# Kernel optimization log

Measured on AMD Instinct MI355X. Metric: run time of the kernel, lower is better.

Reference implementation:

```python
import jax, jax.numpy as jnp
import numpy as np

# dims: batch, time, d_model, d_state, experts, top-k, expert hidden, regime, layers
B, T, D, S, E, K, H, R, L = 4, 512, 384, 32, 6, 2, 512, 5, 2
DI = 2 * D          # d_inner = expand * d_model
DTR = D // 16       # dt_rank = 24


def setup_inputs() -> dict:
    key = jax.random.key(0)
    ks = iter(jax.random.split(key, 48))
    def nrm(shape, s=0.02):
        return jax.random.normal(next(ks), shape, jnp.float32) * s
    inp = {}
    inp["x"] = jax.random.normal(next(ks), (B, T, D), jnp.float32)
    r = jax.random.uniform(next(ks), (B, R), jnp.float32)
    inp["regime"] = r / r.sum(-1, keepdims=True)  # regime posterior
    # FiLM conditioner
    inp["film_w1"] = nrm((R, D)); inp["film_b1"] = jnp.zeros((D,), jnp.float32)
    inp["film_w2"] = nrm((D, 2 * D)); inp["film_b2"] = jnp.zeros((2 * D,), jnp.float32)
    # SelectiveSSMBlock params, stacked over L layers
    inp["ssm_ng"] = jnp.ones((L, D), jnp.float32); inp["ssm_nb"] = jnp.zeros((L, D), jnp.float32)
    inp["in_w"] = nrm((L, D, 2 * DI))
    inp["xp_w"] = nrm((L, DI, DTR + 2 * S))
    inp["dt_w"] = nrm((L, DTR, DI)); inp["dt_b"] = jnp.zeros((L, DI), jnp.float32)
    inp["a_log_real"] = jnp.log(jnp.clip(-0.5 * jax.random.normal(next(ks), (L, DI, S), jnp.float32), 1e-4, None))
    inp["a_imag"] = 0.1 * jax.random.normal(next(ks), (L, DI, S), jnp.float32)
    inp["ssm_d"] = jnp.ones((L, DI), jnp.float32)
    inp["out_w"] = nrm((L, DI, D))
    # MoELayer params, stacked over L layers
    inp["moe_ng"] = jnp.ones((L, D), jnp.float32); inp["moe_nb"] = jnp.zeros((L, D), jnp.float32)
    inp["r_w1"] = nrm((L, D + R, D)); inp["r_b1"] = jnp.zeros((L, D), jnp.float32)
    inp["r_w2"] = nrm((L, D, E)); inp["r_b2"] = jnp.zeros((L, E), jnp.float32)
    inp["e_w1"] = nrm((L, E, D, H)); inp["e_b1"] = jnp.zeros((L, E, H), jnp.float32)
    inp["e_w2"] = nrm((L, E, H, D)); inp["e_b2"] = jnp.zeros((L, E, D), jnp.float32)
    # final norm
    inp["fin_g"] = jnp.ones((D,), jnp.float32); inp["fin_b"] = jnp.zeros((D,), jnp.float32)
    return inp


def _ln(x, g, b):
    m = x.mean(-1, keepdims=True)
    v = ((x - m) ** 2).mean(-1, keepdims=True)
    return (x - m) * jax.lax.rsqrt(v + 1e-5) * g + b


def _ssm_block(h, ng, nb, in_w, xp_w, dt_w, dt_b, alr, aim, d_vec, out_w):
    B_, T_, _ = h.shape
    xn = _ln(h, ng, nb)
    xz = xn @ in_w                        # (B,T,2*DI)
    x_ssm, z = xz[..., :DI], xz[..., DI:]
    x_dbl = x_ssm @ xp_w                  # (B,T,DTR+2S)
    dt = jax.nn.softplus(x_dbl[..., :DTR] @ dt_w + dt_b)   # (B,T,DI)
    Bp = x_dbl[..., DTR:DTR + S]          # (B,T,S)
    Cp = x_dbl[..., DTR + S:]             # (B,T,S)
    A = (-jnp.exp(alr) + 1j * aim).astype(jnp.complex64)   # (DI,S)

    def step(hc, inp):
        dt_t, bt, ct, xt = inp            # (B,DI),(B,S),(B,S),(B,DI)
        dA = jnp.exp(A[None] * dt_t[:, :, None])                       # (B,DI,S) complex
        hc = dA * hc + ((dt_t * xt)[:, :, None] * bt[:, None, :]).astype(jnp.complex64)
        # (h*C).sum(-1).real == (h.real*C).sum(-1) since C is real
        y = jnp.einsum('bds,bs->bd', hc.real, ct)
        return hc, y

    h0 = jnp.zeros((B_, DI, S), jnp.complex64)
    xsT = (jnp.moveaxis(dt, 1, 0), jnp.moveaxis(Bp, 1, 0),
           jnp.moveaxis(Cp, 1, 0), jnp.moveaxis(x_ssm, 1, 0))
    _, ysT = jax.lax.scan(step, h0, xsT)
    y = jnp.moveaxis(ysT, 0, 1) + d_vec * x_ssm   # skip term D*x
    y = y * jax.nn.silu(z)
    return h + y @ out_w                  # residual (dropout=0)


def _moe(h, regime, ng, nb, rw1, rb1, rw2, rb2, ew1, eb1, ew2, eb2):
    xn = _ln(h, ng, nb)
    B_, T_, _ = xn.shape
    reg = jnp.broadcast_to(regime[:, None, :], (B_, T_, R))
    ri = jnp.concatenate([xn, reg], -1)
    gl = jax.nn.silu(ri @ rw1 + rb1) @ rw2 + rb2    # (B,T,E)
    tv, ti = jax.lax.top_k(gl, K)
    tw = jax.nn.softmax(tv, -1)
    eo = jax.nn.silu(jnp.einsum('btd,edh->bteh', xn, ew1) + eb1)
    eo = jnp.einsum('bteh,ehd->bted', eo, ew2) + eb2   # (B,T,E,D)
    sel = jnp.take_along_axis(eo, ti[..., None], axis=2)  # (B,T,K,D)
    out = (sel * tw[..., None]).sum(2)
    gp = jax.nn.softmax(gl, -1)
    avg_p = gp.mean((0, 1))
    avg_m = jax.nn.one_hot(ti[..., 0], E, dtype=gl.dtype).mean((0, 1))
    aux = 0.01 * E * (avg_p * avg_m).sum()
    return h + out, aux


def reference(x, regime, film_w1, film_b1, film_w2, film_b2, ssm_ng, ssm_nb, in_w,
              xp_w, dt_w, dt_b, a_log_real, a_imag, ssm_d, out_w, moe_ng, moe_nb,
              r_w1, r_b1, r_w2, r_b2, e_w1, e_b1, e_w2, e_b2, fin_g, fin_b):
    # FiLM conditioning from regime posterior
    gb = jax.nn.silu(regime @ film_w1 + film_b1) @ film_w2 + film_b2
    gamma, beta = gb[:, :D], gb[:, D:]
    h = x * (gamma[:, None, :] + 1.0) + beta[:, None, :]
    aux = jnp.float32(0.0)
    for l in range(L):
        h = _ssm_block(h, ssm_ng[l], ssm_nb[l], in_w[l], xp_w[l], dt_w[l], dt_b[l],
                       a_log_real[l], a_imag[l], ssm_d[l], out_w[l])
        h, a = _moe(h, regime, moe_ng[l], moe_nb[l], r_w1[l], r_b1[l], r_w2[l], r_b2[l],
                    e_w1[l], e_b1[l], e_w2[l], e_b2[l])
        aux = aux + a
    out = _ln(h, fin_g, fin_b)
    return out, aux
```

## Files before the change

kernel.cpp:

```cpp
#include <hip/hip_runtime.h>
#include <hip/hip_bf16.h>
#include <math.h>

#define B_   4
#define T_   512
#define D_   384
#define S_   32
#define E_   6
#define H_   512
#define R_   5
#define L_   2
#define DI_  768
#define DTR_ 24
#define BT_  2048
#define XPN_ 88
#define SCH  64
#define PIT  40
#define SPD  10
#define SPB  66

typedef short s8v __attribute__((ext_vector_type(8)));
typedef float f32x4 __attribute__((ext_vector_type(4)));
typedef ushort u16x8 __attribute__((ext_vector_type(8)));

__device__ __forceinline__ float siluf(float x) { return x / (1.f + __expf(-x)); }
__device__ __forceinline__ ushort f2b(float f) {
    unsigned u = __float_as_uint(f);
    return (ushort)((u + 0x7FFFu + ((u >> 16) & 1u)) >> 16);
}
__device__ __forceinline__ float b2f(ushort h) { return __uint_as_float(((unsigned)h) << 16); }

#define CN0 1179648L
#define CN1 135168L
#define CN2 36864L
#define CN3 589824L
#define CN4 2359296L
#define CN5 2359296L
#define CN6 294912L
__global__ void conv_k(const float* __restrict__ in_w, const float* __restrict__ xp_w,
                       const float* __restrict__ dt_w, const float* __restrict__ out_w,
                       const float* __restrict__ e_w1, const float* __restrict__ e_w2,
                       const float* __restrict__ r_w1,
                       ushort* __restrict__ in_wb, ushort* __restrict__ xp_wb,
                       ushort* __restrict__ dt_wb, ushort* __restrict__ out_wb,
                       ushort* __restrict__ e1b, ushort* __restrict__ e2b,
                       ushort* __restrict__ r1h, ushort* __restrict__ r1l)
{
    const long total = CN0 + CN1 + CN2 + CN3 + CN4 + CN5 + CN6;
    long stride = (long)gridDim.x * 256;
    for (long i = (long)blockIdx.x * 256 + threadIdx.x; i < total; i += stride) {
        long j = i;
        if (j < CN0) { in_wb[j] = f2b(in_w[j]); continue; }
        j -= CN0;
        if (j < CN1) { xp_wb[j] = f2b(xp_w[j]); continue; }
        j -= CN1;
        if (j < CN2) { dt_wb[j] = f2b(dt_w[j]); continue; }
        j -= CN2;
        if (j < CN3) { out_wb[j] = f2b(out_w[j]); continue; }
        j -= CN3;
        if (j < CN4) { e1b[j] = f2b(e_w1[j]); continue; }
        j -= CN4;
        if (j < CN5) { e2b[j] = f2b(e_w2[j]); continue; }
        j -= CN5;
        {
            long l = j / 147456, rem = j - l * 147456;
            float v = r_w1[l * (long)((D_ + R_) * D_) + rem];
            ushort hv = f2b(v);
            r1h[j] = hv;
            r1l[j] = f2b(v - b2f(hv));
        }
    }
}

__global__ void film_k(const float* __restrict__ regime, const float* __restrict__ w1,
                       const float* __restrict__ b1, const float* __restrict__ w2,
                       const float* __restrict__ b2, float* __restrict__ gb,
                       float* __restrict__ stats)
{
    int b = blockIdx.x;
    int tid = threadIdx.x;
    if (b == 0 && tid < 40) stats[tid] = 0.f;
    __shared__ float t1[D_];
    if (tid < D_) {
        float a = b1[tid];
        for (int r = 0; r < R_; r++) a += regime[b * R_ + r] * w1[r * D_ + tid];
        t1[tid] = siluf(a);
    }
    __syncthreads();
    float a = b2[tid];
    for (int d = 0; d < D_; d++) a += t1[d] * w2[d * (2 * D_) + tid];
    gb[b * (2 * D_) + tid] = a;
}

__global__ void film_apply_k(const float* __restrict__ x, const float* __restrict__ gb,
                             float* __restrict__ h)
{
    int i = blockIdx.x * 256 + threadIdx.x;
    if (i >= B_ * T_ * D_) return;
    int b = i / (T_ * D_);
    int d = i % D_;
    h[i] = x[i] * (1.f + gb[b * (2 * D_) + d]) + gb[b * (2 * D_) + D_ + d];
}

template<int MODE>
__global__ __launch_bounds__(256) void ln_k(const float* __restrict__ in,
                                            const float* __restrict__ g, const float* __restrict__ b,
                                            float* __restrict__ outF,
                                            ushort* __restrict__ outH, ushort* __restrict__ outL)
{
    int row = blockIdx.x;
    int tid = threadIdx.x;
    const float* x = in + (size_t)row * D_;
    float v0 = x[tid];
    float v1 = (tid < D_ - 256) ? x[256 + tid] : 0.f;
    float s = v0 + v1, ss = v0 * v0 + v1 * v1;
#pragma unroll
    for (int o = 32; o > 0; o >>= 1) { s += __shfl_xor(s, o); ss += __shfl_xor(ss, o); }
    __shared__ float sb[8];
    int w = tid >> 6;
    if ((tid & 63) == 0) { sb[w] = s; sb[4 + w] = ss; }
    __syncthreads();
    s = sb[0] + sb[1] + sb[2] + sb[3];
    ss = sb[4] + sb[5] + sb[6] + sb[7];
    float mean = s * (1.f / D_);
    float var = ss * (1.f / D_) - mean * mean;
    float rstd = rsqrtf(var + 1e-5f);
#pragma unroll
    for (int p = 0; p < 2; p++) {
        int c = tid + p * 256;
        if (c >= D_) break;
        float v = (p ? v1 : v0);
        float o = (v - mean) * rstd * g[c] + b[c];
        size_t idx = (size_t)row * D_ + c;
        if (MODE == 0) outF[idx] = o;
        else {
            ushort hv = f2b(o);
            outH[idx] = hv;
            if (MODE == 2) outL[idx] = f2b(o - b2f(hv));
        }
    }
}

template<int MODE>
__global__ __launch_bounds__(256) void selln_k(float* __restrict__ h,
                                               const ushort* __restrict__ eodb,
                                               const float* __restrict__ tw,
                                               const int* __restrict__ tpos,
                                               const float* __restrict__ g, const float* __restrict__ b,
                                               float* __restrict__ outF,
                                               ushort* __restrict__ outH, ushort* __restrict__ outL)
{
    int row = blockIdx.x;
    int tid = threadIdx.x;
    float* hp = h + (size_t)row * D_;
    int p0 = tpos[row * 2], p1 = tpos[row * 2 + 1];
    float w0 = tw[row * 2], w1 = tw[row * 2 + 1];
    const ushort* e0 = eodb + (size_t)p0 * D_;
    const ushort* e1 = eodb + (size_t)p1 * D_;
    float v0 = hp[tid] + w0 * b2f(e0[tid]) + w1 * b2f(e1[tid]);
    float v1 = 0.f;
    if (tid < D_ - 256) v1 = hp[256 + tid] + w0 * b2f(e0[256 + tid]) + w1 * b2f(e1[256 + tid]);
    hp[tid] = v0;
    if (tid < D_ - 256) hp[256 + tid] = v1;
    float s = v0 + v1, ss = v0 * v0 + v1 * v1;
#pragma unroll
    for (int o = 32; o > 0; o >>= 1) { s += __shfl_xor(s, o); ss += __shfl_xor(ss, o); }
    __shared__ float sb[8];
    int w = tid >> 6;
    if ((tid & 63) == 0) { sb[w] = s; sb[4 + w] = ss; }
    __syncthreads();
    s = sb[0] + sb[1] + sb[2] + sb[3];
    ss = sb[4] + sb[5] + sb[6] + sb[7];
    float mean = s * (1.f / D_);
    float var = ss * (1.f / D_) - mean * mean;
    float rstd = rsqrtf(var + 1e-5f);
#pragma unroll
    for (int p = 0; p < 2; p++) {
        int c = tid + p * 256;
        if (c >= D_) break;
        float v = (p ? v1 : v0);
        float o = (v - mean) * rstd * g[c] + b[c];
        size_t idx = (size_t)row * D_ + c;
        if (MODE == 0) outF[idx] = o;
        else {
            ushort hv = f2b(o);
            outH[idx] = hv;
            if (MODE == 2) outL[idx] = f2b(o - b2f(hv));
        }
    }
}

template<int OM, bool NG, bool KG, bool GATHER>
__global__ __launch_bounds__(256) void gemm_b(
    const ushort* __restrict__ A, int lda, long aOff,
    const ushort* __restrict__ W, int ldw, long wOff,
    float* __restrict__ C, int ldc, long cOff,
    ushort* __restrict__ Cb, int ldcb, long cbOff, int nb16,
    const float* __restrict__ bias, long bOff,
    const int* __restrict__ glist, const int* __restrict__ gcnt,
    int N, int K, int act, int acc)
{
    __shared__ __align__(16) ushort As[2][64 * PIT];
    __shared__ __align__(16) ushort Bs[2][64 * PIT];
    const int z = blockIdx.z;
    const int bm = blockIdx.y * 64, bn = blockIdx.x * 64;
    int cnt = 0;
    if (gcnt) { cnt = gcnt[z]; if (bm >= cnt) return; }
    const int tid = threadIdx.x, w = tid >> 6, lane = tid & 63;
    const int wm = (w >> 1) * 32, wn = (w & 1) * 32;
    const int l16 = lane & 15, lk = lane >> 4;
    const int r0 = tid >> 2, c0 = (tid & 3) * 8;
    const ushort* Ab;
    if (GATHER) {
        int gr = bm + r0;
        int t_idx = (gr < cnt) ? glist[(size_t)z * BT_ + gr] : 0;
        Ab = A + (size_t)t_idx * lda;
    } else {
        Ab = A + (size_t)z * aOff + (size_t)(bm + r0) * lda;
    }
    const ushort* Wb = W + (size_t)z * wOff;

    f32x4 accv[2][2];
#pragma unroll
    for (int i = 0; i < 2; i++)
#pragma unroll
        for (int j = 0; j < 2; j++) accv[i][j] = (f32x4)0.f;

    u16x8 arg;
    ushort wrg[8];
    auto LOADA = [&](int k0) {
        arg = *reinterpret_cast<const u16x8*>(Ab + k0 + c0);
    };
    auto LOADW = [&](int k0) {
#pragma unroll
        for (int i = 0; i < 8; i++) {
            int kk = k0 + w * 8 + i;
            bool ok = (!KG || kk < K) && (!NG || (bn + lane) < N);
            wrg[i] = ok ? Wb[(size_t)kk * ldw + bn + lane] : (ushort)0;
        }
    };
    auto STORE = [&](int buf) {
        *reinterpret_cast<u16x8*>(&As[buf][r0 * PIT + c0]) = arg;
        *reinterpret_cast<ushort4*>(&Bs[buf][lane * PIT + w * 8]) =
            make_ushort4(wrg[0], wrg[1], wrg[2], wrg[3]);
        *reinterpret_cast<ushort4*>(&Bs[buf][lane * PIT + w * 8 + 4]) =
            make_ushort4(wrg[4], wrg[5], wrg[6], wrg[7]);
    };

    LOADA(0); LOADW(0); STORE(0);
    __syncthreads();
    const int NIT = (K + 31) / 32;
    for (int it = 0; it < NIT; it++) {
        int cur = it & 1;
        bool more = (it + 1 < NIT);
        if (more) { LOADA((it + 1) * 32); LOADW((it + 1) * 32); }
        s8v af[2], bfr[2];
#pragma unroll
        for (int mf = 0; mf < 2; mf++)
            af[mf] = *reinterpret_cast<const s8v*>(&As[cur][(wm + mf * 16 + l16) * PIT + lk * 8]);
#pragma unroll
        for (int nf = 0; nf < 2; nf++)
            bfr[nf] = *reinterpret_cast<const s8v*>(&Bs[cur][(wn + nf * 16 + l16) * PIT + lk * 8]);
#pragma unroll
        for (int mf = 0; mf < 2; mf++)
#pragma unroll
            for (int nf = 0; nf < 2; nf++)
                accv[mf][nf] = __builtin_amdgcn_mfma_f32_16x16x32_bf16(af[mf], bfr[nf], accv[mf][nf], 0, 0, 0);
        if (more) { STORE(cur ^ 1); __syncthreads(); }
    }

    const float* biasb = bias ? bias + (size_t)z * bOff : nullptr;
#pragma unroll
    for (int mf = 0; mf < 2; mf++) {
#pragma unroll
        for (int nf = 0; nf < 2; nf++) {
            int col = bn + wn + nf * 16 + l16;
            if (NG && col >= N) continue;
#pragma unroll
            for (int r = 0; r < 4; r++) {
                int rr = bm + wm + mf * 16 + lk * 4 + r;
                if (gcnt && rr >= cnt) continue;
                float v = accv[mf][nf][r];
                if (biasb) v += biasb[col];
                if (act == 1) v = siluf(v);
                else if (act == 2) v = (v > 0.f) ? v + log1pf(__expf(-v)) : log1pf(__expf(v));
                if (OM == 0 || OM == 2) {
                    float* Cz = C + (size_t)z * cOff;
                    size_t ci = (size_t)rr * ldc + col;
                    Cz[ci] = acc ? (Cz[ci] + v) : v;
                }
                if (OM == 1 || OM == 2) {
                    if (col < nb16)
                        (Cb + (size_t)z * cbOff)[(size_t)rr * ldcb + col] = f2b(v);
                }
                if (OM == 3) {
                    if (col < nb16)
                        Cb[(size_t)rr * ldcb + col] = f2b(v);
                    if (col >= 24) {
                        int q = col - 24;
                        C[(size_t)rr * 64 + ((q < 32) ? (2 * q) : (2 * (q - 32) + 1))] = v;
                    }
                }
            }
        }
    }
}

__global__ __launch_bounds__(256) void gemm3_k(
    const ushort* __restrict__ Ah, const ushort* __restrict__ Al, int lda,
    const ushort* __restrict__ Wh, const ushort* __restrict__ Wl, int ldw,
    float* __restrict__ C,
    const float* __restrict__ bias,
    const float* __restrict__ regime, const float* __restrict__ rw1t,
    int N, int K)
{
    __shared__ __align__(16) ushort sAh[64 * PIT], sAl[64 * PIT];
    __shared__ __align__(16) ushort sWh[128 * PIT], sWl[128 * PIT];
    const int bm = blockIdx.y * 64, bn = blockIdx.x * 128;
    const int tid = threadIdx.x, w = tid >> 6, lane = tid & 63;
    const int wm = (w >> 1) * 32, wn = (w & 1) * 64;
    const int l16 = lane & 15, lk = lane >> 4;
    const int r0 = tid >> 2, c0 = (tid & 3) * 8;
    f32x4 accv[2][4];
#pragma unroll
    for (int i = 0; i < 2; i++)
#pragma unroll
        for (int j = 0; j < 4; j++) accv[i][j] = (f32x4)0.f;

    for (int k0 = 0; k0 < K; k0 += 32) {
        *reinterpret_cast<u16x8*>(&sAh[r0 * PIT + c0]) =
            *reinterpret_cast<const u16x8*>(Ah + (size_t)(bm + r0) * lda + k0 + c0);
        *reinterpret_cast<u16x8*>(&sAl[r0 * PIT + c0]) =
            *reinterpret_cast<const u16x8*>(Al + (size_t)(bm + r0) * lda + k0 + c0);
#pragma unroll
        for (int hh = 0; hh < 2; hh++) {
            int n = hh * 64 + lane;
            ushort th[8], tl[8];
#pragma unroll
            for (int i = 0; i < 8; i++) {
                int kk = k0 + w * 8 + i;
                th[i] = Wh[(size_t)kk * ldw + bn + n];
                tl[i] = Wl[(size_t)kk * ldw + bn + n];
            }
            *reinterpret_cast<ushort4*>(&sWh[n * PIT + w * 8])     = make_ushort4(th[0], th[1], th[2], th[3]);
            *reinterpret_cast<ushort4*>(&sWh[n * PIT + w * 8 + 4]) = make_ushort4(th[4], th[5], th[6], th[7]);
            *reinterpret_cast<ushort4*>(&sWl[n * PIT + w * 8])     = make_ushort4(tl[0], tl[1], tl[2], tl[3]);
            *reinterpret_cast<ushort4*>(&sWl[n * PIT + w * 8 + 4]) = make_ushort4(tl[4], tl[5], tl[6], tl[7]);
        }
        __syncthreads();
        s8v ah[2], al[2], bh[4], bl[4];
#pragma unroll
        for (int mf = 0; mf < 2; mf++) {
            ah[mf] = *reinterpret_cast<const s8v*>(&sAh[(wm + mf * 16 + l16) * PIT + lk * 8]);
            al[mf] = *reinterpret_cast<const s8v*>(&sAl[(wm + mf * 16 + l16) * PIT + lk * 8]);
        }
#pragma unroll
        for (int nf = 0; nf < 4; nf++) {
            bh[nf] = *reinterpret_cast<const s8v*>(&sWh[(wn + nf * 16 + l16) * PIT + lk * 8]);
            bl[nf] = *reinterpret_cast<const s8v*>(&sWl[(wn + nf * 16 + l16) * PIT + lk * 8]);
        }
#pragma unroll
        for (int mf = 0; mf < 2; mf++)
#pragma unroll
            for (int nf = 0; nf < 4; nf++) {
                accv[mf][nf] = __builtin_amdgcn_mfma_f32_16x16x32_bf16(ah[mf], bh[nf], accv[mf][nf], 0, 0, 0);
                accv[mf][nf] = __builtin_amdgcn_mfma_f32_16x16x32_bf16(ah[mf], bl[nf], accv[mf][nf], 0, 0, 0);
                accv[mf][nf] = __builtin_amdgcn_mfma_f32_16x16x32_bf16(al[mf], bh[nf], accv[mf][nf], 0, 0, 0);
            }
        __syncthreads();
    }
    const float* rg = regime + (bm / T_) * R_;
#pragma unroll
    for (int mf = 0; mf < 2; mf++)
#pragma unroll
        for (int nf = 0; nf < 4; nf++) {
            int col = bn + wn + nf * 16 + l16;
            float rb = 0.f;
#pragma unroll
            for (int r = 0; r < R_; r++) rb += rg[r] * rw1t[r * D_ + col];
#pragma unroll
            for (int r = 0; r < 4; r++) {
                int rr = bm + wm + mf * 16 + lk * 4 + r;
                float v = accv[mf][nf][r] + bias[col] + rb;
                C[(size_t)rr * N + col] = siluf(v);
            }
        }
}

__global__ __launch_bounds__(128) void scan_k(
    const float* __restrict__ xz, const ushort* __restrict__ xdblb,
    const float* __restrict__ bcint,
    const float* __restrict__ dt_w, const float* __restrict__ dt_b,
    const float* __restrict__ alr, const float* __restrict__ aim,
    const float* __restrict__ dvecp, ushort* __restrict__ ygb)
{
    int p = blockIdx.x;
    int blk = (p & 7) * 96 + (p >> 3);
    int b = blk / 192;
    int dbase = (blk % 192) * 4;
    int tid = threadIdx.x;
    int ch = tid >> 5;
    int s = tid & 31;
    int d = dbase + ch;
    __shared__ __align__(16) float sdx[64 * SPD];
    __shared__ __align__(16) float sbc[64 * SPB];
    __shared__ float sacc[SCH * 4][33];
    int cch = tid & 3;
    float wdt[24];
#pragma unroll
    for (int k = 0; k < 24; k++) wdt[k] = dt_w[k * DI_ + dbase + cch];
    float dtbias = dt_b[dbase + cch];

    float negA = -__expf(alr[d * S_ + s]);
    float aimv = aim[d * S_ + s];
    float4 dv4 = *reinterpret_cast<const float4*>(dvecp + dbase);
    float dvc[4] = {dv4.x, dv4.y, dv4.z, dv4.w};
    float hre = 0.f, him = 0.f;
    const float* xzp = xz + (size_t)b * T_ * (2 * DI_);
    const ushort* xdp = xdblb + (size_t)b * T_ * 32;
    const float* bcp = bcint + (size_t)b * T_ * 64;
    ushort* ygp = ygb + (size_t)b * T_ * DI_;

    for (int c = 0; c < T_ / SCH; c++) {
        int tc = c * SCH;
        __syncthreads();
        if (tid < 64) {
            int t = tid;
            float4 x4 = *reinterpret_cast<const float4*>(xzp + (size_t)(tc + t) * (2 * DI_) + dbase);
            sdx[t * SPD + 1] = x4.x;
            sdx[t * SPD + 3] = x4.y;
            sdx[t * SPD + 5] = x4.z;
            sdx[t * SPD + 7] = x4.w;
        }
        {
            int t0 = tid >> 2;
#pragma unroll
            for (int j = 0; j < 2; j++) {
                int t = t0 + j * 32;
                const ushort* xr = xdp + (size_t)(tc + t) * 32;
                u16x8 a0 = *reinterpret_cast<const u16x8*>(xr);
                u16x8 a1 = *reinterpret_cast<const u16x8*>(xr + 8);
                u16x8 a2 = *reinterpret_cast<const u16x8*>(xr + 16);
                float acc = dtbias;
#pragma unroll
                for (int k = 0; k < 8; k++) acc = fmaf(b2f((ushort)a0[k]), wdt[k], acc);
#pragma unroll
                for (int k = 0; k < 8; k++) acc = fmaf(b2f((ushort)a1[k]), wdt[8 + k], acc);
#pragma unroll
                for (int k = 0; k < 8; k++) acc = fmaf(b2f((ushort)a2[k]), wdt[16 + k], acc);
                float dtv = (acc > 0.f) ? acc + log1pf(__expf(-acc)) : log1pf(__expf(acc));
                sdx[t * SPD + 2 * cch] = dtv;
            }
        }
#pragma unroll
        for (int i = 0; i < 8; i++) {
            int idx = tid + i * 128;
            int tt = idx >> 4, q = idx & 15;
            *reinterpret_cast<float4*>(&sbc[tt * SPB + 4 * q]) =
                *reinterpret_cast<const float4*>(bcp + (size_t)(tc + tt) * 64 + 4 * q);
        }
        __syncthreads();

        const float* dxr = &sdx[2 * ch];
        const float* bcr = &sbc[2 * s];
        float2 dx0 = *reinterpret_cast<const float2*>(dxr);
        float2 bc0 = *reinterpret_cast<const float2*>(bcr);
        float2 dx1 = *reinterpret_cast<const float2*>(dxr + SPD);
        float2 bc1 = *reinterpret_cast<const float2*>(bcr + SPB);
#pragma unroll 4
        for (int t = 0; t < SCH; t++) {
            float2 dx2 = make_float2(0.f, 0.f), bc2 = dx2;
            if (t + 2 < SCH) {
                dx2 = *reinterpret_cast<const float2*>(dxr + (t + 2) * SPD);
                bc2 = *reinterpret_cast<const float2*>(bcr + (t + 2) * SPB);
            }
            float e = __expf(negA * dx0.x);
            float sn, cs;
            __sincosf(aimv * dx0.x, &sn, &cs);
            float dre = e * cs, dim = e * sn;
            float u = dx0.x * dx0.y * bc0.x;
            float nre = fmaf(dre, hre, fmaf(-dim, him, u));
            him = fmaf(dre, him, dim * hre);
            hre = nre;
            sacc[t * 4 + ch][s] = hre * bc0.y;
            dx0 = dx1; bc0 = bc1; dx1 = dx2; bc1 = bc2;
        }
        __syncthreads();

#pragma unroll
        for (int p2 = 0; p2 < 2; p2++) {
            int r = tid + p2 * 128;
            int t = r >> 2, c4 = r & 3;
            float acc = 0.f;
#pragma unroll
            for (int s2 = 0; s2 < 32; s2++) acc += sacc[r][s2];
            float xv = sdx[t * SPD + 2 * c4 + 1];
            float zv = xzp[(size_t)(tc + t) * (2 * DI_) + DI_ + dbase + c4];
            float y = (acc + dvc[c4] * xv) * siluf(zv);
            ygp[(size_t)(tc + t) * DI_ + dbase + c4] = f2b(y);
        }
    }
}

__global__ __launch_bounds__(256) void gl_k(const float* __restrict__ hmid,
                                            const float* __restrict__ rw2l,
                                            const float* __restrict__ rb2l, float* __restrict__ gl)
{
    int pid = blockIdx.x * 16 + (threadIdx.x >> 4);
    int li = threadIdx.x & 15;
    int t = pid / E_, e = pid - t * E_;
    const float* hp = hmid + (size_t)t * D_;
    float a = 0.f;
#pragma unroll 4
    for (int j = 0; j < D_ / 16; j++) {
        int k = li + j * 16;
        a += hp[k] * rw2l[k * E_ + e];
    }
#pragma unroll
    for (int o = 8; o > 0; o >>= 1) a += __shfl_xor(a, o, 16);
    if (li == 0) gl[t * E_ + e] = a + rb2l[e];
}

__global__ __launch_bounds__(1024) void router_assign_k(const float* __restrict__ gl,
                                                        float* __restrict__ tw,
                                                        int* __restrict__ glist,
                                                        int* __restrict__ tpos,
                                                        int* __restrict__ cnt,
                                                        float* __restrict__ statL)
{
    __shared__ float s_p[E_], s_c[E_];
    __shared__ int scnt[E_];
    int tid = threadIdx.x;
    if (tid < E_) { s_p[tid] = 0.f; s_c[tid] = 0.f; scnt[tid] = 0; }
    __syncthreads();
    float lp[E_] = {0.f, 0.f, 0.f, 0.f, 0.f, 0.f};
    float lc[E_] = {0.f, 0.f, 0.f, 0.f, 0.f, 0.f};
    for (int t = tid; t < BT_; t += 1024) {
        float g[E_];
        for (int e = 0; e < E_; e++) g[e] = gl[t * E_ + e];
        int i0 = 0; float v0 = g[0];
        for (int e = 1; e < E_; e++) if (g[e] > v0) { v0 = g[e]; i0 = e; }
        int i1 = -1; float v1 = -1e30f;
        for (int e = 0; e < E_; e++) if (e != i0 && g[e] > v1) { v1 = g[e]; i1 = e; }
        if (i1 < 0) i1 = (i0 == 0) ? 1 : 0;
        float e1 = __expf(v1 - v0);
        float inv = 1.f / (1.f + e1);
        tw[t * 2] = inv; tw[t * 2 + 1] = e1 * inv;
        int pos0 = atomicAdd(&scnt[i0], 1);
        glist[i0 * BT_ + pos0] = t;
        tpos[2 * t] = i0 * BT_ + pos0;
        int pos1 = atomicAdd(&scnt[i1], 1);
        glist[i1 * BT_ + pos1] = t;
        tpos[2 * t + 1] = i1 * BT_ + pos1;
        float pb[E_], se = 0.f;
        for (int e = 0; e < E_; e++) { pb[e] = __expf(g[e] - v0); se += pb[e]; }
        float rse = 1.f / se;
#pragma unroll
        for (int e = 0; e < E_; e++) {
            lp[e] += pb[e] * rse;
            lc[e] += (i0 == e) ? 1.f : 0.f;
        }
    }
#pragma unroll
    for (int e = 0; e < E_; e++) {
        float v = lp[e], u = lc[e];
#pragma unroll
        for (int o = 32; o > 0; o >>= 1) { v += __shfl_xor(v, o); u += __shfl_xor(u, o); }
        if ((tid & 63) == 0) { atomicAdd(&s_p[e], v); atomicAdd(&s_c[e], u); }
    }
    __syncthreads();
    if (tid < E_) {
        cnt[tid] = scnt[tid];
        statL[tid] = s_p[tid];
        statL[8 + tid] = s_c[tid];
    }
}

__global__ void write_aux_k(const float* __restrict__ stats, float* __restrict__ out)
{
    if (threadIdx.x == 0 && blockIdx.x == 0) {
        float aux = 0.f;
        for (int l = 0; l < L_; l++) {
            float s = 0.f;
            for (int e = 0; e < E_; e++) s += stats[l * 16 + e] * stats[l * 16 + 8 + e];
            aux += 0.01f * (float)E_ * s / ((float)BT_ * (float)BT_);
        }
        out[BT_ * D_] = aux;
    }
}

extern "C" void kernel_launch(void* const* d_in, const int* in_sizes, int n_in,
                              void* d_out, int out_size, void* d_ws, size_t ws_size,
                              hipStream_t stream)
{
    const float* x       = (const float*)d_in[0];
    const float* regime  = (const float*)d_in[1];
    const float* film_w1 = (const float*)d_in[2];
    const float* film_b1 = (const float*)d_in[3];
    const float* film_w2 = (const float*)d_in[4];
    const float* film_b2 = (const float*)d_in[5];
    const float* ssm_ng  = (const float*)d_in[6];
    const float* ssm_nb  = (const float*)d_in[7];
    const float* in_w    = (const float*)d_in[8];
    const float* xp_w    = (const float*)d_in[9];
    const float* dt_w    = (const float*)d_in[10];
    const float* dt_b    = (const float*)d_in[11];
    const float* alr     = (const float*)d_in[12];
    const float* aimp    = (const float*)d_in[13];
    const float* ssm_d   = (const float*)d_in[14];
    const float* out_w   = (const float*)d_in[15];
    const float* moe_ng  = (const float*)d_in[16];
    const float* moe_nb  = (const float*)d_in[17];
    const float* r_w1    = (const float*)d_in[18];
    const float* r_b1    = (const float*)d_in[19];
    const float* r_w2    = (const float*)d_in[20];
    const float* r_b2    = (const float*)d_in[21];
    const float* e_w1    = (const float*)d_in[22];
    const float* e_b1    = (const float*)d_in[23];
    const float* e_w2    = (const float*)d_in[24];
    const float* e_b2    = (const float*)d_in[25];
    const float* fin_g   = (const float*)d_in[26];
    const float* fin_b   = (const float*)d_in[27];

    float* ws = (float*)d_ws;
    size_t o = 0;
    float*  h      = ws + o; o += 786432;
    float*  stats  = ws + o; o += 64;
    ushort* xnH    = (ushort*)(ws + o); o += 393216;
    ushort* xnL    = (ushort*)(ws + o); o += 393216;
    float*  gl     = ws + o; o += 12288;
    float*  tw     = ws + o; o += 4096;
    int*    glist  = (int*)(ws + o); o += 12288;
    int*    tpos   = (int*)(ws + o); o += 4096;
    int*    cnt    = (int*)(ws + o); o += 16;
    ushort* in_wb  = (ushort*)(ws + o); o += 589824;
    ushort* xp_wb  = (ushort*)(ws + o); o += 67584;
    ushort* dt_wb  = (ushort*)(ws + o); o += 18432;
    ushort* out_wb = (ushort*)(ws + o); o += 294912;
    ushort* e1b    = (ushort*)(ws + o); o += 1179648;
    ushort* e2b    = (ushort*)(ws + o); o += 1179648;
    ushort* r1h    = (ushort*)(ws + o); o += 147456;
    ushort* r1l    = (ushort*)(ws + o); o += 147456;
    float*  xz    = ws + o;
    ushort* xzb   = (ushort*)(ws + o + 3145728);
    ushort* xdblb = (ushort*)(ws + o + 3932160);
    float*  bcint = ws + o + 3964928;
    ushort* ygb   = (ushort*)(ws + o + 4096000);
    float*  hmid  = ws + o;
    ushort* eohb  = (ushort*)(ws + o + 786432);
    ushort* eodb  = (ushort*)(ws + o + 3932160);
    float*  gb    = ws + o;

    conv_k<<<2048, 256, 0, stream>>>(in_w, xp_w, dt_w, out_w, e_w1, e_w2, r_w1,
                                     in_wb, xp_wb, dt_wb, out_wb, e1b, e2b, r1h, r1l);
    film_k<<<B_, 2 * D_, 0, stream>>>(regime, film_w1, film_b1, film_w2, film_b2, gb, stats);
    film_apply_k<<<(B_ * T_ * D_ + 255) / 256, 256, 0, stream>>>(x, gb, h);

    for (int l = 0; l < L_; l++) {
        if (l == 0)
            ln_k<1><<<BT_, 256, 0, stream>>>(h, ssm_ng, ssm_nb, nullptr, xnH, nullptr);
        gemm_b<2, false, false, false><<<dim3(24, 32), 256, 0, stream>>>(
            xnH, D_, 0, in_wb + (size_t)l * 589824, 2 * DI_, 0,
            xz, 2 * DI_, 0, xzb, DI_, 0, DI_,
            nullptr, 0, nullptr, nullptr, 2 * DI_, D_, 0, 0);
        gemm_b<3, true, false, false><<<dim3(2, 32), 256, 0, stream>>>(
            xzb, DI_, 0, xp_wb + (size_t)l * 67584, XPN_, 0,
            bcint, 64, 0, xdblb, 32, 0, 32,
            nullptr, 0, nullptr, nullptr, XPN_, DI_, 0, 0);
        scan_k<<<B_ * 192, 128, 0, stream>>>(
            xz, xdblb, bcint,
            dt_w + (size_t)l * DTR_ * DI_, dt_b + l * DI_,
            alr + (size_t)l * DI_ * S_, aimp + (size_t)l * DI_ * S_,
            ssm_d + l * DI_, ygb);
        gemm_b<0, false, false, false><<<dim3(6, 32), 256, 0, stream>>>(
            ygb, DI_, 0, out_wb + (size_t)l * 294912, D_, 0,
            h, D_, 0, nullptr, 0, 0, 0,
            nullptr, 0, nullptr, nullptr, D_, DI_, 0, 1);

        ln_k<2><<<BT_, 256, 0, stream>>>(h, moe_ng + l * D_, moe_nb + l * D_, nullptr, xnH, xnL);
        gemm3_k<<<dim3(3, 32), 256, 0, stream>>>(
            xnH, xnL, D_, r1h + (size_t)l * 147456, r1l + (size_t)l * 147456, D_,
            hmid, r_b1 + l * D_,
            regime, r_w1 + (size_t)l * ((D_ + R_) * D_) + (size_t)D_ * D_,
            D_, D_);
        gl_k<<<BT_ * E_ / 16, 256, 0, stream>>>(hmid, r_w2 + (size_t)l * D_ * E_, r_b2 + l * E_, gl);
        router_assign_k<<<1, 1024, 0, stream>>>(gl, tw, glist, tpos, cnt, stats + l * 16);
        gemm_b<1, false, false, true><<<dim3(8, 32, 6), 256, 0, stream>>>(
            xnH, D_, 0, e1b + (size_t)l * 1179648, H_, (long)D_ * H_,
            nullptr, 0, 0, eohb, H_, (long)BT_ * H_, H_,
            e_b1 + (size_t)l * E_ * H_, H_, glist, cnt, H_, D_, 1, 0);
        gemm_b<1, false, false, false><<<dim3(6, 32, 6), 256, 0, stream>>>(
            eohb, H_, (long)BT_ * H_, e2b + (size_t)l * 1179648, D_, (long)H_ * D_,
            nullptr, 0, 0, eodb, D_, (long)BT_ * D_, D_,
            e_b2 + (size_t)l * E_ * D_, D_, nullptr, cnt, D_, H_, 0, 0);
        if (l < L_ - 1)
            selln_k<1><<<BT_, 256, 0, stream>>>(h, eodb, tw, tpos,
                ssm_ng + (l + 1) * D_, ssm_nb + (l + 1) * D_, nullptr, xnH, nullptr);
        else
            selln_k<0><<<BT_, 256, 0, stream>>>(h, eodb, tw, tpos,
                fin_g, fin_b, (float*)d_out, nullptr, nullptr);
    }

    write_aux_k<<<1, 64, 0, stream>>>(stats, (float*)d_out);
}
```

Before: 489.6 us.

## Fuse router logits GEMM into router hidden GEMM epilogue and stage z in scan

The router's second projection (hidden to expert logits) is folded into gemm3_k's epilogue. Each block now computes a 64-column partial dot product with r_w2 from shared memory and writes one of six partial logit slices, which router_assign_k sums together with the bias. This removes the hmid round trip through global memory and the separate gl_k launch, and doubles the gemm3 grid via smaller N tiles. Separately, the scan kernel now stages the z gate values in shared memory alongside x, replacing scattered global reads in the output loop. The cost is extra partial-sum traffic and a small per-block serial dot loop in the epilogue.

Measured after the change: 478.2 us. 1.02x faster.

```diff
diff --git a/kernel.cpp b/kernel.cpp
--- a/kernel.cpp
+++ b/kernel.cpp
@@ -16,7 +16,7 @@
 #define XPN_ 88
 #define SCH  64
 #define PIT  40
-#define SPD  10
+#define SPD  12
 #define SPB  66
 
 typedef short s8v __attribute__((ext_vector_type(8)));
@@ -309,60 +309,60 @@
 __global__ __launch_bounds__(256) void gemm3_k(
     const ushort* __restrict__ Ah, const ushort* __restrict__ Al, int lda,
     const ushort* __restrict__ Wh, const ushort* __restrict__ Wl, int ldw,
-    float* __restrict__ C,
     const float* __restrict__ bias,
     const float* __restrict__ regime, const float* __restrict__ rw1t,
-    int N, int K)
+    const float* __restrict__ rw2l,
+    float* __restrict__ glp,
+    int K)
 {
     __shared__ __align__(16) ushort sAh[64 * PIT], sAl[64 * PIT];
-    __shared__ __align__(16) ushort sWh[128 * PIT], sWl[128 * PIT];
-    const int bm = blockIdx.y * 64, bn = blockIdx.x * 128;
+    __shared__ __align__(16) ushort sWh[64 * PIT], sWl[64 * PIT];
+    __shared__ __align__(16) float sV[64 * 66];
+    const int bm = blockIdx.y * 64, bn = blockIdx.x * 64;
     const int tid = threadIdx.x, w = tid >> 6, lane = tid & 63;
-    const int wm = (w >> 1) * 32, wn = (w & 1) * 64;
+    const int wm = (w >> 1) * 32, wn = (w & 1) * 32;
     const int l16 = lane & 15, lk = lane >> 4;
     const int r0 = tid >> 2, c0 = (tid & 3) * 8;
-    f32x4 accv[2][4];
+    f32x4 accv[2][2];
 #pragma unroll
     for (int i = 0; i < 2; i++)
 #pragma unroll
-        for (int j = 0; j < 4; j++) accv[i][j] = (f32x4)0.f;
+        for (int j = 0; j < 2; j++) accv[i][j] = (f32x4)0.f;
 
     for (int k0 = 0; k0 < K; k0 += 32) {
         *reinterpret_cast<u16x8*>(&sAh[r0 * PIT + c0]) =
             *reinterpret_cast<const u16x8*>(Ah + (size_t)(bm + r0) * lda + k0 + c0);
         *reinterpret_cast<u16x8*>(&sAl[r0 * PIT + c0]) =
             *reinterpret_cast<const u16x8*>(Al + (size_t)(bm + r0) * lda + k0 + c0);
-#pragma unroll
-        for (int hh = 0; hh < 2; hh++) {
-            int n = hh * 64 + lane;
+        {
             ushort th[8], tl[8];
 #pragma unroll
             for (int i = 0; i < 8; i++) {
                 int kk = k0 + w * 8 + i;
-                th[i] = Wh[(size_t)kk * ldw + bn + n];
-                tl[i] = Wl[(size_t)kk * ldw + bn + n];
+                th[i] = Wh[(size_t)kk * ldw + bn + lane];
+                tl[i] = Wl[(size_t)kk * ldw + bn + lane];
             }
-            *reinterpret_cast<ushort4*>(&sWh[n * PIT + w * 8])     = make_ushort4(th[0], th[1], th[2], th[3]);
-            *reinterpret_cast<ushort4*>(&sWh[n * PIT + w * 8 + 4]) = make_ushort4(th[4], th[5], th[6], th[7]);
-            *reinterpret_cast<ushort4*>(&sWl[n * PIT + w * 8])     = make_ushort4(tl[0], tl[1], tl[2], tl[3]);
-            *reinterpret_cast<ushort4*>(&sWl[n * PIT + w * 8 + 4]) = make_ushort4(tl[4], tl[5], tl[6], tl[7]);
+            *reinterpret_cast<ushort4*>(&sWh[lane * PIT + w * 8])     = make_ushort4(th[0], th[1], th[2], th[3]);
+            *reinterpret_cast<ushort4*>(&sWh[lane * PIT + w * 8 + 4]) = make_ushort4(th[4], th[5], th[6], th[7]);
+            *reinterpret_cast<ushort4*>(&sWl[lane * PIT + w * 8])     = make_ushort4(tl[0], tl[1], tl[2], tl[3]);
+            *reinterpret_cast<ushort4*>(&sWl[lane * PIT + w * 8 + 4]) = make_ushort4(tl[4], tl[5], tl[6], tl[7]);
         }
         __syncthreads();
-        s8v ah[2], al[2], bh[4], bl[4];
+        s8v ah[2], al[2], bh[2], bl[2];
 #pragma unroll
         for (int mf = 0; mf < 2; mf++) {
             ah[mf] = *reinterpret_cast<const s8v*>(&sAh[(wm + mf * 16 + l16) * PIT + lk * 8]);
             al[mf] = *reinterpret_cast<const s8v*>(&sAl[(wm + mf * 16 + l16) * PIT + lk * 8]);
         }
 #pragma unroll
-        for (int nf = 0; nf < 4; nf++) {
+        for (int nf = 0; nf < 2; nf++) {
             bh[nf] = *reinterpret_cast<const s8v*>(&sWh[(wn + nf * 16 + l16) * PIT + lk * 8]);
             bl[nf] = *reinterpret_cast<const s8v*>(&sWl[(wn + nf * 16 + l16) * PIT + lk * 8]);
         }
 #pragma unroll
         for (int mf = 0; mf < 2; mf++)
 #pragma unroll
-            for (int nf = 0; nf < 4; nf++) {
+            for (int nf = 0; nf < 2; nf++) {
                 accv[mf][nf] = __builtin_amdgcn_mfma_f32_16x16x32_bf16(ah[mf], bh[nf], accv[mf][nf], 0, 0, 0);
                 accv[mf][nf] = __builtin_amdgcn_mfma_f32_16x16x32_bf16(ah[mf], bl[nf], accv[mf][nf], 0, 0, 0);
                 accv[mf][nf] = __builtin_amdgcn_mfma_f32_16x16x32_bf16(al[mf], bh[nf], accv[mf][nf], 0, 0, 0);
@@ -371,20 +371,28 @@
     }
     const float* rg = regime + (bm / T_) * R_;
 #pragma unroll
-    for (int mf = 0; mf < 2; mf++)
-#pragma unroll
-        for (int nf = 0; nf < 4; nf++) {
-            int col = bn + wn + nf * 16 + l16;
-            float rb = 0.f;
-#pragma unroll
-            for (int r = 0; r < R_; r++) rb += rg[r] * rw1t[r * D_ + col];
+    for (int nf = 0; nf < 2; nf++) {
+        int col = bn + wn + nf * 16 + l16;
+        float rb = bias[col - bn + bn];
+#pragma unroll
+        for (int r = 0; r < R_; r++) rb += rg[r] * rw1t[r * D_ + col];
+#pragma unroll
+        for (int mf = 0; mf < 2; mf++)
 #pragma unroll
             for (int r = 0; r < 4; r++) {
-                int rr = bm + wm + mf * 16 + lk * 4 + r;
-                float v = accv[mf][nf][r] + bias[col] + rb;
-                C[(size_t)rr * N + col] = siluf(v);
+                int rr = wm + mf * 16 + lk * 4 + r;
+                sV[rr * 66 + (col - bn)] = siluf(accv[mf][nf][r] + rb);
             }
-        }
+    }
+    __syncthreads();
+    for (int job = tid; job < 64 * E_; job += 256) {
+        int row = job / E_, e = job - row * E_;
+        float a = 0.f;
+#pragma unroll 8
+        for (int c = 0; c < 64; c++)
+            a += sV[row * 66 + c] * rw2l[(size_t)(bn + c) * E_ + e];
+        glp[(size_t)blockIdx.x * (BT_ * E_) + (size_t)(bm + row) * E_ + e] = a;
+    }
 }
 
 __global__ __launch_bounds__(128) void scan_k(
@@ -427,10 +435,15 @@
         if (tid < 64) {
             int t = tid;
             float4 x4 = *reinterpret_cast<const float4*>(xzp + (size_t)(tc + t) * (2 * DI_) + dbase);
+            float4 z4 = *reinterpret_cast<const float4*>(xzp + (size_t)(tc + t) * (2 * DI_) + DI_ + dbase);
             sdx[t * SPD + 1] = x4.x;
             sdx[t * SPD + 3] = x4.y;
             sdx[t * SPD + 5] = x4.z;
             sdx[t * SPD + 7] = x4.w;
+            sdx[t * SPD + 8]  = z4.x;
+            sdx[t * SPD + 9]  = z4.y;
+            sdx[t * SPD + 10] = z4.z;
+            sdx[t * SPD + 11] = z4.w;
         }
         {
             int t0 = tid >> 2;
@@ -495,33 +508,15 @@
 #pragma unroll
             for (int s2 = 0; s2 < 32; s2++) acc += sacc[r][s2];
             float xv = sdx[t * SPD + 2 * c4 + 1];
-            float zv = xzp[(size_t)(tc + t) * (2 * DI_) + DI_ + dbase + c4];
+            float zv = sdx[t * SPD + 8 + c4];
             float y = (acc + dvc[c4] * xv) * siluf(zv);
             ygp[(size_t)(tc + t) * DI_ + dbase + c4] = f2b(y);
         }
     }
 }
 
-__global__ __launch_bounds__(256) void gl_k(const float* __restrict__ hmid,
-                                            const float* __restrict__ rw2l,
-                                            const float* __restrict__ rb2l, float* __restrict__ gl)
-{
-    int pid = blockIdx.x * 16 + (threadIdx.x >> 4);
-    int li = threadIdx.x & 15;
-    int t = pid / E_, e = pid - t * E_;
-    const float* hp = hmid + (size_t)t * D_;
-    float a = 0.f;
-#pragma unroll 4
-    for (int j = 0; j < D_ / 16; j++) {
-        int k = li + j * 16;
-        a += hp[k] * rw2l[k * E_ + e];
-    }
-#pragma unroll
-    for (int o = 8; o > 0; o >>= 1) a += __shfl_xor(a, o, 16);
-    if (li == 0) gl[t * E_ + e] = a + rb2l[e];
-}
-
-__global__ __launch_bounds__(1024) void router_assign_k(const float* __restrict__ gl,
+__global__ __launch_bounds__(1024) void router_assign_k(const float* __restrict__ glp,
+                                                        const float* __restrict__ rb2l,
                                                         float* __restrict__ tw,
                                                         int* __restrict__ glist,
                                                         int* __restrict__ tpos,
@@ -537,7 +532,12 @@
     float lc[E_] = {0.f, 0.f, 0.f, 0.f, 0.f, 0.f};
     for (int t = tid; t < BT_; t += 1024) {
         float g[E_];
-        for (int e = 0; e < E_; e++) g[e] = gl[t * E_ + e];
+        for (int e = 0; e < E_; e++) {
+            float a = rb2l[e];
+#pragma unroll
+            for (int j = 0; j < 6; j++) a += glp[(size_t)j * (BT_ * E_) + t * E_ + e];
+            g[e] = a;
+        }
         int i0 = 0; float v0 = g[0];
         for (int e = 1; e < E_; e++) if (g[e] > v0) { v0 = g[e]; i0 = e; }
         int i1 = -1; float v1 = -1e30f;
@@ -628,7 +628,7 @@
     float*  stats  = ws + o; o += 64;
     ushort* xnH    = (ushort*)(ws + o); o += 393216;
     ushort* xnL    = (ushort*)(ws + o); o += 393216;
-    float*  gl     = ws + o; o += 12288;
+    float*  glp    = ws + o; o += 73728;
     float*  tw     = ws + o; o += 4096;
     int*    glist  = (int*)(ws + o); o += 12288;
     int*    tpos   = (int*)(ws + o); o += 4096;
@@ -646,7 +646,6 @@
     ushort* xdblb = (ushort*)(ws + o + 3932160);
     float*  bcint = ws + o + 3964928;
     ushort* ygb   = (ushort*)(ws + o + 4096000);
-    float*  hmid  = ws + o;
     ushort* eohb  = (ushort*)(ws + o + 786432);
     ushort* eodb  = (ushort*)(ws + o + 3932160);
     float*  gb    = ws + o;
@@ -678,13 +677,13 @@
             nullptr, 0, nullptr, nullptr, D_, DI_, 0, 1);
 
         ln_k<2><<<BT_, 256, 0, stream>>>(h, moe_ng + l * D_, moe_nb + l * D_, nullptr, xnH, xnL);
-        gemm3_k<<<dim3(3, 32), 256, 0, stream>>>(
+        gemm3_k<<<dim3(6, 32), 256, 0, stream>>>(
             xnH, xnL, D_, r1h + (size_t)l * 147456, r1l + (size_t)l * 147456, D_,
-            hmid, r_b1 + l * D_,
+            r_b1 + l * D_,
             regime, r_w1 + (size_t)l * ((D_ + R_) * D_) + (size_t)D_ * D_,
-            D_, D_);
-        gl_k<<<BT_ * E_ / 16, 256, 0, stream>>>(hmid, r_w2 + (size_t)l * D_ * E_, r_b2 + l * E_, gl);
-        router_assign_k<<<1, 1024, 0, stream>>>(gl, tw, glist, tpos, cnt, stats + l * 16);
+            r_w2 + (size_t)l * D_ * E_,
+            glp, D_);
+        router_assign_k<<<1, 1024, 0, stream>>>(glp, r_b2 + l * E_, tw, glist, tpos, cnt, stats + l * 16);
         gemm_b<1, false, false, true><<<dim3(8, 32, 6), 256, 0, stream>>>(
             xnH, D_, 0, e1b + (size_t)l * 1179648, H_, (long)D_ * H_,
             nullptr, 0, 0, eohb, H_, (long)BT_ * H_, H_,
```
